# Kernel optimization log

Measured on AMD Instinct MI355X. Metric: run time of the kernel, lower is better.

## Reference

```python
import jax, jax.numpy as jnp
import numpy as np

N = 50000
E = 800000
IN, HID, OUT = 128, 128, 64


def setup_inputs() -> dict:
    key = jax.random.key(0)
    ks = jax.random.split(key, 12)
    x = jax.random.normal(ks[0], (N, IN), dtype=jnp.float32)
    src = jax.random.randint(ks[1], (E,), 0, N)
    dst = jax.random.randint(ks[2], (E,), 0, N)
    edge_index = jnp.stack([src, dst]).astype(jnp.int64)
    def lin(k, fan_in, fan_out):
        s = 1.0 / np.sqrt(fan_in)
        return jax.random.uniform(k, (fan_in, fan_out), jnp.float32, -s, s)
    return {
        "x": x,
        "edge_index": edge_index,
        "w_l0": lin(ks[3], IN, HID), "b0": jnp.zeros((HID,), jnp.float32), "w_r0": lin(ks[4], IN, HID),
        "w_l1": lin(ks[5], HID, HID), "b1": jnp.zeros((HID,), jnp.float32), "w_r1": lin(ks[6], HID, HID),
        "w_l2": lin(ks[7], HID, OUT), "b2": jnp.zeros((OUT,), jnp.float32), "w_r2": lin(ks[8], HID, OUT),
    }


def _sage_conv(x, src, dst, w_l, b, w_r, num_nodes):
    # mean aggregation of source features onto destination nodes
    msg = x[src]                                            # [E, d]
    summed = jax.ops.segment_sum(msg, dst, num_segments=num_nodes)  # [N, d]
    deg = jax.ops.segment_sum(jnp.ones((src.shape[0],), x.dtype), dst, num_segments=num_nodes)
    aggr = summed / jnp.maximum(deg, 1.0)[:, None]
    # out = lin_l(aggr) + lin_r(x_root); bias only on lin_l (PyG SAGEConv default)
    return aggr @ w_l + b + x @ w_r


def reference(x, edge_index, w_l0, b0, w_r0, w_l1, b1, w_r1, w_l2, b2, w_r2):
    src, dst = edge_index[0].astype(jnp.int32), edge_index[1].astype(jnp.int32)
    n = x.shape[0]
    h = jax.nn.relu(_sage_conv(x, src, dst, w_l0, b0, w_r0, n))  # dropout: eval mode -> identity
    h = jax.nn.relu(_sage_conv(h, src, dst, w_l1, b1, w_r1, n))
    return _sage_conv(h, src, dst, w_l2, b2, w_r2, n)
```

## Files before the change

kernel.cpp:

```cpp
#include <hip/hip_runtime.h>
#include <cstdint>
#include <cstddef>


#define HID 128
#define NSLICE 8
#define FILL_BLOCKS_PER_SLICE 256
#define FILL_BLOCKS (NSLICE * FILL_BLOCKS_PER_SLICE)
#define GEMM_BLOCKS 1024
#define CAP 64

using short8 = __attribute__((ext_vector_type(8))) short;
using f32x4  = __attribute__((ext_vector_type(4))) float;


__device__ __forceinline__ unsigned short f32_to_bf16(float f)
{
    union { float f; unsigned int i; } c; c.f = f;
    const unsigned int x = c.i;
    const unsigned int r = x + 0x7fffu + ((x >> 16) & 1u);
    return (unsigned short)(r >> 16);
}

__device__ __forceinline__ float bf16_hi_to_f32(unsigned int hi16_in_low)
{
    union { unsigned int i; float f; } c; c.i = hi16_in_low << 16;
    return c.f;
}

__device__ __forceinline__ unsigned int pack_bf16(float a, float b)
{
    return ((unsigned int)f32_to_bf16(b) << 16) | (unsigned int)f32_to_bf16(a);
}


#define PREP_THREADS (2 * 2 * HID * HID + 2 * 64 * HID)

__global__ __launch_bounds__(256) void prep_wt_zero_kernel(
    const float* __restrict__ wl0, const float* __restrict__ wr0,
    const float* __restrict__ wl1, const float* __restrict__ wr1,
    const float* __restrict__ wl2, const float* __restrict__ wr2,
    unsigned short* __restrict__ wt0, unsigned short* __restrict__ wt1,
    unsigned short* __restrict__ wt2, int* __restrict__ deg, int n)
{
    const int idx = blockIdx.x * 256 + threadIdx.x;
    const int per128 = 2 * HID * HID;
    if (idx < per128) {
        const int k = idx & (HID - 1), c = idx >> 7;
        const float v = (c < HID) ? wl0[(size_t)k * HID + c] : wr0[(size_t)k * HID + (c - HID)];
        wt0[idx] = f32_to_bf16(v);
    } else if (idx < 2 * per128) {
        const int j = idx - per128;
        const int k = j & (HID - 1), c = j >> 7;
        const float v = (c < HID) ? wl1[(size_t)k * HID + c] : wr1[(size_t)k * HID + (c - HID)];
        wt1[j] = f32_to_bf16(v);
    } else if (idx < PREP_THREADS) {
        const int j = idx - 2 * per128;
        const int k = j & (HID - 1), c = j >> 7;
        const float v = (c < 64) ? wl2[(size_t)k * 64 + c] : wr2[(size_t)k * 64 + (c - 64)];
        wt2[j] = f32_to_bf16(v);
    } else {
        const int j = idx - PREP_THREADS;
        if (j < n) deg[j] = 0;
    }
}


__global__ __launch_bounds__(256) void bucket_fill_sliced_kernel(
    const int* __restrict__ src, const int* __restrict__ dst,
    int* __restrict__ deg, unsigned short* __restrict__ esrc, int E, int n)
{
    const int slice = blockIdx.x & (NSLICE - 1);
    const int nps   = (n + NSLICE - 1) / NSLICE;
    const int lo    = slice * nps;
    const unsigned span = (unsigned)(min(lo + nps, n) - lo);
    const int stride = FILL_BLOCKS_PER_SLICE * 256;
    const int nq = E >> 2;

    for (int q = (blockIdx.x >> 3) * 256 + threadIdx.x; q < nq; q += stride) {
        const int4 d4 = ((const int4*)dst)[q];
        const bool p0 = (unsigned)(d4.x - lo) < span;
        const bool p1 = (unsigned)(d4.y - lo) < span;
        const bool p2 = (unsigned)(d4.z - lo) < span;
        const bool p3 = (unsigned)(d4.w - lo) < span;
        if (p0 | p1 | p2 | p3) {
            const int4 s4 = ((const int4*)src)[q];
            if (p0 && (unsigned)s4.x < (unsigned)n) {
                const int p = atomicAdd(&deg[d4.x], 1);
                if (p < CAP) esrc[(size_t)d4.x * CAP + p] = (unsigned short)s4.x;
            }
            if (p1 && (unsigned)s4.y < (unsigned)n) {
                const int p = atomicAdd(&deg[d4.y], 1);
                if (p < CAP) esrc[(size_t)d4.y * CAP + p] = (unsigned short)s4.y;
            }
            if (p2 && (unsigned)s4.z < (unsigned)n) {
                const int p = atomicAdd(&deg[d4.z], 1);
                if (p < CAP) esrc[(size_t)d4.z * CAP + p] = (unsigned short)s4.z;
            }
            if (p3 && (unsigned)s4.w < (unsigned)n) {
                const int p = atomicAdd(&deg[d4.w], 1);
                if (p < CAP) esrc[(size_t)d4.w * CAP + p] = (unsigned short)s4.w;
            }
        }
    }
    if ((blockIdx.x >> 3) == 0 && slice == 0) {
        for (int e = (nq << 2) + threadIdx.x; e < E; e += 256) {
            const int d = dst[e];
            const int s = src[e];
            if ((unsigned)d < (unsigned)n && (unsigned)s < (unsigned)n) {
                const int p = atomicAdd(&deg[d], 1);
                if (p < CAP) esrc[(size_t)d * CAP + p] = (unsigned short)s;
            }
        }
    }
}


template <int DOUT, bool IN_F32, bool R_BF16>
__global__ __launch_bounds__(256) void sage_mfma_gemm(
    const void* __restrict__ hin,
    const unsigned short* __restrict__ wtc,
    const float* __restrict__ bias,
    unsigned short* __restrict__ p, void* __restrict__ r, int n)
{
    constexpr int CPW = (2 * DOUT) / 64;

    const int tx   = threadIdx.x;
    const int wv   = tx >> 6;
    const int lane = tx & 63;
    const int quad = lane >> 4;
    const int l15  = lane & 15;

    short8 B[CPW][4];
#pragma unroll
    for (int t = 0; t < CPW; ++t) {
        const int c = (wv * CPW + t) * 16 + l15;
#pragma unroll
        for (int q = 0; q < 4; ++q)
            B[t][q] = *(const short8*)(wtc + (size_t)c * HID + q * 32 + quad * 8);
    }

    const int slabs = (n + 15) >> 4;
    for (int slab = blockIdx.x; slab < slabs; slab += gridDim.x) {
        const int r0 = slab * 16;
        const int rr = min(r0 + l15, n - 1);

        short8 A[4];
        if (IN_F32) {
            const float* hf = (const float*)hin;
#pragma unroll
            for (int q = 0; q < 4; ++q) {
                const float4 f0 = *(const float4*)(hf + (size_t)rr * HID + q * 32 + quad * 8);
                const float4 f1 = *(const float4*)(hf + (size_t)rr * HID + q * 32 + quad * 8 + 4);
                short8 a;
                a[0] = (short)f32_to_bf16(f0.x); a[1] = (short)f32_to_bf16(f0.y);
                a[2] = (short)f32_to_bf16(f0.z); a[3] = (short)f32_to_bf16(f0.w);
                a[4] = (short)f32_to_bf16(f1.x); a[5] = (short)f32_to_bf16(f1.y);
                a[6] = (short)f32_to_bf16(f1.z); a[7] = (short)f32_to_bf16(f1.w);
                A[q] = a;
            }
        } else {
            const unsigned short* hb = (const unsigned short*)hin;
#pragma unroll
            for (int q = 0; q < 4; ++q)
                A[q] = *(const short8*)(hb + (size_t)rr * HID + q * 32 + quad * 8);
        }

        f32x4 acc[CPW];
#pragma unroll
        for (int t = 0; t < CPW; ++t) acc[t] = (f32x4){0.f, 0.f, 0.f, 0.f};
#pragma unroll
        for (int q = 0; q < 4; ++q)
#pragma unroll
            for (int t = 0; t < CPW; ++t)
                acc[t] = __builtin_amdgcn_mfma_f32_16x16x32_bf16(A[q], B[t][q], acc[t], 0, 0, 0);

#pragma unroll
        for (int t = 0; t < CPW; ++t) {
            const int c0  = (wv * CPW + t) * 16;
            const int col = c0 + l15;
            if (c0 < DOUT) {
#pragma unroll
                for (int i = 0; i < 4; ++i) {
                    const int row = r0 + quad * 4 + i;
                    if (row < n) p[(size_t)row * DOUT + col] = f32_to_bf16(acc[t][i]);
                }
            } else {
                const float bv = bias[col - DOUT];
#pragma unroll
                for (int i = 0; i < 4; ++i) {
                    const int row = r0 + quad * 4 + i;
                    if (row < n) {
                        const float v = acc[t][i] + bv;
                        if (R_BF16)
                            ((unsigned short*)r)[(size_t)row * DOUT + (col - DOUT)] = f32_to_bf16(v);
                        else
                            ((float*)r)[(size_t)row * DOUT + (col - DOUT)] = v;
                    }
                }
            }
        }
    }
}


template <int DOUT, bool RELU, bool OUTBF16, bool R_BF16>
__global__ __launch_bounds__(256) void sage_post_aggregate(
    const unsigned short* __restrict__ p, const void* __restrict__ r,
    const int* __restrict__ deg, const unsigned short* __restrict__ esrc,
    void* __restrict__ out, int n)
{
    const int wid  = threadIdx.x >> 6;
    const int lane = threadIdx.x & 63;
    const int node = blockIdx.x * 4 + wid;
    if (node >= n) return;
    const int dg   = deg[node];
    const int degc = min(dg, CAP);
    const float inv = 1.0f / fmaxf((float)dg, 1.0f);

    const int sidx = (int)esrc[(size_t)node * CAP + lane];

    if constexpr (DOUT == 128) {
        const int g  = lane >> 4;
        const int lo = lane & 15;
        float acc[4][8];
#pragma unroll
        for (int j = 0; j < 4; ++j)
#pragma unroll
            for (int c = 0; c < 8; ++c) acc[j][c] = 0.f;

        for (int e0 = 0; e0 < degc; e0 += 16) {
#pragma unroll
            for (int j = 0; j < 4; ++j) {
                const int slot = e0 + j * 4 + g;
                const float w  = (slot < degc) ? 1.0f : 0.0f;
                const int s    = __shfl(sidx, min(slot, degc - 1), 64);
                const short8 v = *(const short8*)(p + (size_t)s * DOUT + lo * 8);
#pragma unroll
                for (int c = 0; c < 8; ++c)
                    acc[j][c] = fmaf(w, bf16_hi_to_f32((unsigned short)v[c]), acc[j][c]);
            }
        }
        float s8[8];
#pragma unroll
        for (int c = 0; c < 8; ++c) {
            float t = (acc[0][c] + acc[1][c]) + (acc[2][c] + acc[3][c]);
            t += __shfl_xor(t, 16, 64);
            t += __shfl_xor(t, 32, 64);
            s8[c] = t * inv;
        }
        if (g == 0) {
            float rc[8];
            if (R_BF16) {
                const short8 rv = *(const short8*)((const unsigned short*)r + (size_t)node * DOUT + lo * 8);
#pragma unroll
                for (int c = 0; c < 8; ++c) rc[c] = bf16_hi_to_f32((unsigned short)rv[c]);
            } else {
                const float4 q0 = *(const float4*)((const float*)r + (size_t)node * DOUT + lo * 8);
                const float4 q1 = *(const float4*)((const float*)r + (size_t)node * DOUT + lo * 8 + 4);
                rc[0] = q0.x; rc[1] = q0.y; rc[2] = q0.z; rc[3] = q0.w;
                rc[4] = q1.x; rc[5] = q1.y; rc[6] = q1.z; rc[7] = q1.w;
            }
            float o[8];
#pragma unroll
            for (int c = 0; c < 8; ++c) {
                o[c] = s8[c] + rc[c];
                if (RELU) o[c] = fmaxf(o[c], 0.f);
            }
            if (OUTBF16) {
                uint4 st;
                st.x = pack_bf16(o[0], o[1]); st.y = pack_bf16(o[2], o[3]);
                st.z = pack_bf16(o[4], o[5]); st.w = pack_bf16(o[6], o[7]);
                *(uint4*)((unsigned short*)out + (size_t)node * DOUT + lo * 8) = st;
            } else {
                float4 s0, s1;
                s0.x = o[0]; s0.y = o[1]; s0.z = o[2]; s0.w = o[3];
                s1.x = o[4]; s1.y = o[5]; s1.z = o[6]; s1.w = o[7];
                *(float4*)((float*)out + (size_t)node * DOUT + lo * 8) = s0;
                *(float4*)((float*)out + (size_t)node * DOUT + lo * 8 + 4) = s1;
            }
        }
    } else {
        const int g  = lane >> 3;
        const int lo = lane & 7;
        float acc[2][8];
#pragma unroll
        for (int j = 0; j < 2; ++j)
#pragma unroll
            for (int c = 0; c < 8; ++c) acc[j][c] = 0.f;

        for (int e0 = 0; e0 < degc; e0 += 16) {
#pragma unroll
            for (int j = 0; j < 2; ++j) {
                const int slot = e0 + j * 8 + g;
                const float w  = (slot < degc) ? 1.0f : 0.0f;
                const int s    = __shfl(sidx, min(slot, degc - 1), 64);
                const short8 v = *(const short8*)(p + (size_t)s * DOUT + lo * 8);
#pragma unroll
                for (int c = 0; c < 8; ++c)
                    acc[j][c] = fmaf(w, bf16_hi_to_f32((unsigned short)v[c]), acc[j][c]);
            }
        }
        float s8[8];
#pragma unroll
        for (int c = 0; c < 8; ++c) {
            float t = acc[0][c] + acc[1][c];
            t += __shfl_xor(t, 8, 64);
            t += __shfl_xor(t, 16, 64);
            t += __shfl_xor(t, 32, 64);
            s8[c] = t * inv;
        }
        if (g == 0) {
            float rc[8];
            if (R_BF16) {
                const short8 rv = *(const short8*)((const unsigned short*)r + (size_t)node * DOUT + lo * 8);
#pragma unroll
                for (int c = 0; c < 8; ++c) rc[c] = bf16_hi_to_f32((unsigned short)rv[c]);
            } else {
                const float4 q0 = *(const float4*)((const float*)r + (size_t)node * DOUT + lo * 8);
                const float4 q1 = *(const float4*)((const float*)r + (size_t)node * DOUT + lo * 8 + 4);
                rc[0] = q0.x; rc[1] = q0.y; rc[2] = q0.z; rc[3] = q0.w;
                rc[4] = q1.x; rc[5] = q1.y; rc[6] = q1.z; rc[7] = q1.w;
            }
            float o[8];
#pragma unroll
            for (int c = 0; c < 8; ++c) {
                o[c] = s8[c] + rc[c];
                if (RELU) o[c] = fmaxf(o[c], 0.f);
            }
            if (OUTBF16) {
                uint4 st;
                st.x = pack_bf16(o[0], o[1]); st.y = pack_bf16(o[2], o[3]);
                st.z = pack_bf16(o[4], o[5]); st.w = pack_bf16(o[6], o[7]);
                *(uint4*)((unsigned short*)out + (size_t)node * DOUT + lo * 8) = st;
            } else {
                float4 s0, s1;
                s0.x = o[0]; s0.y = o[1]; s0.z = o[2]; s0.w = o[3];
                s1.x = o[4]; s1.y = o[5]; s1.z = o[6]; s1.w = o[7];
                *(float4*)((float*)out + (size_t)node * DOUT + lo * 8) = s0;
                *(float4*)((float*)out + (size_t)node * DOUT + lo * 8 + 4) = s1;
            }
        }
    }
}


static inline size_t align_up(size_t v, size_t a) { return (v + a - 1) & ~(a - 1); }

extern "C" void kernel_launch(void* const* d_in, const int* in_sizes, int n_in,
                              void* d_out, int out_size, void* d_ws, size_t ws_size,
                              hipStream_t stream)
{
    const float* x   = (const float*)d_in[0];
    const int*   ei  = (const int*)d_in[1];
    const float* wl0 = (const float*)d_in[2];
    const float* b0  = (const float*)d_in[3];
    const float* wr0 = (const float*)d_in[4];
    const float* wl1 = (const float*)d_in[5];
    const float* b1  = (const float*)d_in[6];
    const float* wr1 = (const float*)d_in[7];
    const float* wl2 = (const float*)d_in[8];
    const float* b2  = (const float*)d_in[9];
    const float* wr2 = (const float*)d_in[10];
    float*       out = (float*)d_out;

    const int N = in_sizes[0] / HID;
    const int E = in_sizes[1] / 2;
    const int* src = ei;
    const int* dst = ei + E;

    char*  ws  = (char*)d_ws;
    size_t off = 0;
    int* deg      = (int*)(ws + off); off = align_up(off + (size_t)N * 4, 256);
    unsigned short* esrc = (unsigned short*)(ws + off); off = align_up(off + (size_t)N * CAP * 2, 256);
    unsigned short* pbuf = (unsigned short*)(ws + off); off = align_up(off + (size_t)N * HID * 2, 256);
    unsigned short* rb16 = (unsigned short*)(ws + off); off = align_up(off + (size_t)N * HID * 2, 256);
    float* rbf32  = (float*)(ws + off); off = align_up(off + (size_t)N * HID * 4, 256);
    unsigned short* hbf = (unsigned short*)(ws + off); off = align_up(off + (size_t)N * HID * 2, 256);
    unsigned short* wt0 = (unsigned short*)(ws + off); off = align_up(off + (size_t)2 * HID * HID * 2, 256);
    unsigned short* wt1 = (unsigned short*)(ws + off); off = align_up(off + (size_t)2 * HID * HID * 2, 256);
    unsigned short* wt2 = (unsigned short*)(ws + off); off = align_up(off + (size_t)HID * HID * 2, 256);
    (void)ws_size; (void)n_in; (void)out_size;

    prep_wt_zero_kernel<<<(PREP_THREADS + N + 255) / 256, 256, 0, stream>>>(
        wl0, wr0, wl1, wr1, wl2, wr2, wt0, wt1, wt2, deg, N);

    bucket_fill_sliced_kernel<<<FILL_BLOCKS, 256, 0, stream>>>(
        src, dst, deg, esrc, E, N);

    const int aggGrid = (N + 3) / 4;

    sage_mfma_gemm<128, true, true><<<GEMM_BLOCKS, 256, 0, stream>>>(x, wt0, b0, pbuf, rb16, N);
    sage_post_aggregate<128, true, true, true><<<aggGrid, 256, 0, stream>>>(pbuf, rb16, deg, esrc, hbf, N);

    sage_mfma_gemm<128, false, true><<<GEMM_BLOCKS, 256, 0, stream>>>(hbf, wt1, b1, pbuf, rb16, N);
    sage_post_aggregate<128, true, true, true><<<aggGrid, 256, 0, stream>>>(pbuf, rb16, deg, esrc, hbf, N);

    sage_mfma_gemm<64, false, false><<<GEMM_BLOCKS, 256, 0, stream>>>(hbf, wt2, b2, pbuf, rbf32, N);
    sage_post_aggregate<64, false, false, false><<<aggGrid, 256, 0, stream>>>(pbuf, rbf32, deg, esrc, out, N);
}
```

Before: 285.2 us.

## Fuse the three SAGE layers into one cooperative persistent kernel with grid syncs

Replaces the six separate GEMM and aggregation launches with a single cooperative kernel. The kernel runs the gemm and aggregate bodies as grid-stride loops and separates the stages with grid.sync(). This removes five kernel launch gaps and tail effects. In exchange, the grid is capped by occupancy (at most 2048 blocks), so the aggregation, which used 12500 blocks, loses parallelism and latency hiding, and every grid barrier adds its own cost. A fallback to the original launches is kept for when the cooperative launch fails.

After: 678.9 us. +138.0%, slower.

```diff
diff --git a/kernel.cpp b/kernel.cpp
--- a/kernel.cpp
+++ b/kernel.cpp
@@ -1,6 +1,9 @@
 #include <hip/hip_runtime.h>
+#include <hip/hip_cooperative_groups.h>
 #include <cstdint>
 #include <cstddef>
+
+namespace cg = cooperative_groups;
 
 
 #define HID 128
@@ -117,9 +120,9 @@
 
 
 template <int DOUT, bool IN_F32, bool R_BF16>
-__global__ __launch_bounds__(256) void sage_mfma_gemm(
-    const void* __restrict__ hin,
-    const unsigned short* __restrict__ wtc,
+__device__ __forceinline__ void gemm_body(
+    int bid, int nblk,
+    const void* __restrict__ hin, const unsigned short* __restrict__ wtc,
     const float* __restrict__ bias,
     unsigned short* __restrict__ p, void* __restrict__ r, int n)
 {
@@ -141,7 +144,7 @@
     }
 
     const int slabs = (n + 15) >> 4;
-    for (int slab = blockIdx.x; slab < slabs; slab += gridDim.x) {
+    for (int slab = bid; slab < slabs; slab += nblk) {
         const int r0 = slab * 16;
         const int rr = min(r0 + l15, n - 1);
 
@@ -203,6 +206,157 @@
     }
 }
 
+template <int DOUT, bool IN_F32, bool R_BF16>
+__global__ __launch_bounds__(256) void sage_mfma_gemm(
+    const void* __restrict__ hin, const unsigned short* __restrict__ wtc,
+    const float* __restrict__ bias,
+    unsigned short* __restrict__ p, void* __restrict__ r, int n)
+{
+    gemm_body<DOUT, IN_F32, R_BF16>(blockIdx.x, gridDim.x, hin, wtc, bias, p, r, n);
+}
+
+
+template <int DOUT, bool RELU, bool OUTBF16, bool R_BF16>
+__device__ __forceinline__ void agg_body(
+    int bid, int nblk,
+    const unsigned short* __restrict__ p, const void* __restrict__ r,
+    const int* __restrict__ deg, const unsigned short* __restrict__ esrc,
+    void* __restrict__ out, int n)
+{
+    const int wid  = threadIdx.x >> 6;
+    const int lane = threadIdx.x & 63;
+
+    for (int node = bid * 4 + wid; node < n; node += nblk * 4) {
+        const int dg   = deg[node];
+        const int degc = min(dg, CAP);
+        const float inv = 1.0f / fmaxf((float)dg, 1.0f);
+
+        const int sidx = (int)esrc[(size_t)node * CAP + lane];
+
+        if constexpr (DOUT == 128) {
+            const int g  = lane >> 4;
+            const int lo = lane & 15;
+            float acc[4][8];
+#pragma unroll
+            for (int j = 0; j < 4; ++j)
+#pragma unroll
+                for (int c = 0; c < 8; ++c) acc[j][c] = 0.f;
+
+            for (int e0 = 0; e0 < degc; e0 += 16) {
+#pragma unroll
+                for (int j = 0; j < 4; ++j) {
+                    const int slot = e0 + j * 4 + g;
+                    const float w  = (slot < degc) ? 1.0f : 0.0f;
+                    const int s    = __shfl(sidx, min(slot, degc - 1), 64);
+                    const short8 v = *(const short8*)(p + (size_t)s * DOUT + lo * 8);
+#pragma unroll
+                    for (int c = 0; c < 8; ++c)
+                        acc[j][c] = fmaf(w, bf16_hi_to_f32((unsigned short)v[c]), acc[j][c]);
+                }
+            }
+            float s8[8];
+#pragma unroll
+            for (int c = 0; c < 8; ++c) {
+                float t = (acc[0][c] + acc[1][c]) + (acc[2][c] + acc[3][c]);
+                t += __shfl_xor(t, 16, 64);
+                t += __shfl_xor(t, 32, 64);
+                s8[c] = t * inv;
+            }
+            if (g == 0) {
+                float rc[8];
+                if (R_BF16) {
+                    const short8 rv = *(const short8*)((const unsigned short*)r + (size_t)node * DOUT + lo * 8);
+#pragma unroll
+                    for (int c = 0; c < 8; ++c) rc[c] = bf16_hi_to_f32((unsigned short)rv[c]);
+                } else {
+                    const float4 q0 = *(const float4*)((const float*)r + (size_t)node * DOUT + lo * 8);
+                    const float4 q1 = *(const float4*)((const float*)r + (size_t)node * DOUT + lo * 8 + 4);
+                    rc[0] = q0.x; rc[1] = q0.y; rc[2] = q0.z; rc[3] = q0.w;
+                    rc[4] = q1.x; rc[5] = q1.y; rc[6] = q1.z; rc[7] = q1.w;
+                }
+                float o[8];
+#pragma unroll
+                for (int c = 0; c < 8; ++c) {
+                    o[c] = s8[c] + rc[c];
+                    if (RELU) o[c] = fmaxf(o[c], 0.f);
+                }
+                if (OUTBF16) {
+                    uint4 st;
+                    st.x = pack_bf16(o[0], o[1]); st.y = pack_bf16(o[2], o[3]);
+                    st.z = pack_bf16(o[4], o[5]); st.w = pack_bf16(o[6], o[7]);
+                    *(uint4*)((unsigned short*)out + (size_t)node * DOUT + lo * 8) = st;
+                } else {
+                    float4 s0, s1;
+                    s0.x = o[0]; s0.y = o[1]; s0.z = o[2]; s0.w = o[3];
+                    s1.x = o[4]; s1.y = o[5]; s1.z = o[6]; s1.w = o[7];
+                    *(float4*)((float*)out + (size_t)node * DOUT + lo * 8) = s0;
+                    *(float4*)((float*)out + (size_t)node * DOUT + lo * 8 + 4) = s1;
+                }
+            }
+        } else {
+            const int g  = lane >> 3;
+            const int lo = lane & 7;
+            float acc[2][8];
+#pragma unroll
+            for (int j = 0; j < 2; ++j)
+#pragma unroll
+                for (int c = 0; c < 8; ++c) acc[j][c] = 0.f;
+
+            for (int e0 = 0; e0 < degc; e0 += 16) {
+#pragma unroll
+                for (int j = 0; j < 2; ++j) {
+                    const int slot = e0 + j * 8 + g;
+                    const float w  = (slot < degc) ? 1.0f : 0.0f;
+                    const int s    = __shfl(sidx, min(slot, degc - 1), 64);
+                    const short8 v = *(const short8*)(p + (size_t)s * DOUT + lo * 8);
+#pragma unroll
+                    for (int c = 0; c < 8; ++c)
+                        acc[j][c] = fmaf(w, bf16_hi_to_f32((unsigned short)v[c]), acc[j][c]);
+                }
+            }
+            float s8[8];
+#pragma unroll
+            for (int c = 0; c < 8; ++c) {
+                float t = acc[0][c] + acc[1][c];
+                t += __shfl_xor(t, 8, 64);
+                t += __shfl_xor(t, 16, 64);
+                t += __shfl_xor(t, 32, 64);
+                s8[c] = t * inv;
+            }
+            if (g == 0) {
+                float rc[8];
+                if (R_BF16) {
+                    const short8 rv = *(const short8*)((const unsigned short*)r + (size_t)node * DOUT + lo * 8);
+#pragma unroll
+                    for (int c = 0; c < 8; ++c) rc[c] = bf16_hi_to_f32((unsigned short)rv[c]);
+                } else {
+                    const float4 q0 = *(const float4*)((const float*)r + (size_t)node * DOUT + lo * 8);
+                    const float4 q1 = *(const float4*)((const float*)r + (size_t)node * DOUT + lo * 8 + 4);
+                    rc[0] = q0.x; rc[1] = q0.y; rc[2] = q0.z; rc[3] = q0.w;
+                    rc[4] = q1.x; rc[5] = q1.y; rc[6] = q1.z; rc[7] = q1.w;
+                }
+                float o[8];
+#pragma unroll
+                for (int c = 0; c < 8; ++c) {
+                    o[c] = s8[c] + rc[c];
+                    if (RELU) o[c] = fmaxf(o[c], 0.f);
+                }
+                if (OUTBF16) {
+                    uint4 st;
+                    st.x = pack_bf16(o[0], o[1]); st.y = pack_bf16(o[2], o[3]);
+                    st.z = pack_bf16(o[4], o[5]); st.w = pack_bf16(o[6], o[7]);
+                    *(uint4*)((unsigned short*)out + (size_t)node * DOUT + lo * 8) = st;
+                } else {
+                    float4 s0, s1;
+                    s0.x = o[0]; s0.y = o[1]; s0.z = o[2]; s0.w = o[3];
+                    s1.x = o[4]; s1.y = o[5]; s1.z = o[6]; s1.w = o[7];
+                    *(float4*)((float*)out + (size_t)node * DOUT + lo * 8) = s0;
+                    *(float4*)((float*)out + (size_t)node * DOUT + lo * 8 + 4) = s1;
+                }
+            }
+        }
+    }
+}
 
 template <int DOUT, bool RELU, bool OUTBF16, bool R_BF16>
 __global__ __launch_bounds__(256) void sage_post_aggregate(
@@ -210,138 +364,35 @@
     const int* __restrict__ deg, const unsigned short* __restrict__ esrc,
     void* __restrict__ out, int n)
 {
-    const int wid  = threadIdx.x >> 6;
-    const int lane = threadIdx.x & 63;
-    const int node = blockIdx.x * 4 + wid;
-    if (node >= n) return;
-    const int dg   = deg[node];
-    const int degc = min(dg, CAP);
-    const float inv = 1.0f / fmaxf((float)dg, 1.0f);
-
-    const int sidx = (int)esrc[(size_t)node * CAP + lane];
-
-    if constexpr (DOUT == 128) {
-        const int g  = lane >> 4;
-        const int lo = lane & 15;
-        float acc[4][8];
-#pragma unroll
-        for (int j = 0; j < 4; ++j)
-#pragma unroll
-            for (int c = 0; c < 8; ++c) acc[j][c] = 0.f;
-
-        for (int e0 = 0; e0 < degc; e0 += 16) {
-#pragma unroll
-            for (int j = 0; j < 4; ++j) {
-                const int slot = e0 + j * 4 + g;
-                const float w  = (slot < degc) ? 1.0f : 0.0f;
-                const int s    = __shfl(sidx, min(slot, degc - 1), 64);
-                const short8 v = *(const short8*)(p + (size_t)s * DOUT + lo * 8);
-#pragma unroll
-                for (int c = 0; c < 8; ++c)
-                    acc[j][c] = fmaf(w, bf16_hi_to_f32((unsigned short)v[c]), acc[j][c]);
-            }
-        }
-        float s8[8];
-#pragma unroll
-        for (int c = 0; c < 8; ++c) {
-            float t = (acc[0][c] + acc[1][c]) + (acc[2][c] + acc[3][c]);
-            t += __shfl_xor(t, 16, 64);
-            t += __shfl_xor(t, 32, 64);
-            s8[c] = t * inv;
-        }
-        if (g == 0) {
-            float rc[8];
-            if (R_BF16) {
-                const short8 rv = *(const short8*)((const unsigned short*)r + (size_t)node * DOUT + lo * 8);
-#pragma unroll
-                for (int c = 0; c < 8; ++c) rc[c] = bf16_hi_to_f32((unsigned short)rv[c]);
-            } else {
-                const float4 q0 = *(const float4*)((const float*)r + (size_t)node * DOUT + lo * 8);
-                const float4 q1 = *(const float4*)((const float*)r + (size_t)node * DOUT + lo * 8 + 4);
-                rc[0] = q0.x; rc[1] = q0.y; rc[2] = q0.z; rc[3] = q0.w;
-                rc[4] = q1.x; rc[5] = q1.y; rc[6] = q1.z; rc[7] = q1.w;
-            }
-            float o[8];
-#pragma unroll
-            for (int c = 0; c < 8; ++c) {
-                o[c] = s8[c] + rc[c];
-                if (RELU) o[c] = fmaxf(o[c], 0.f);
-            }
-            if (OUTBF16) {
-                uint4 st;
-                st.x = pack_bf16(o[0], o[1]); st.y = pack_bf16(o[2], o[3]);
-                st.z = pack_bf16(o[4], o[5]); st.w = pack_bf16(o[6], o[7]);
-                *(uint4*)((unsigned short*)out + (size_t)node * DOUT + lo * 8) = st;
-            } else {
-                float4 s0, s1;
-                s0.x = o[0]; s0.y = o[1]; s0.z = o[2]; s0.w = o[3];
-                s1.x = o[4]; s1.y = o[5]; s1.z = o[6]; s1.w = o[7];
-                *(float4*)((float*)out + (size_t)node * DOUT + lo * 8) = s0;
-                *(float4*)((float*)out + (size_t)node * DOUT + lo * 8 + 4) = s1;
-            }
-        }
-    } else {
-        const int g  = lane >> 3;
-        const int lo = lane & 7;
-        float acc[2][8];
-#pragma unroll
-        for (int j = 0; j < 2; ++j)
-#pragma unroll
-            for (int c = 0; c < 8; ++c) acc[j][c] = 0.f;
-
-        for (int e0 = 0; e0 < degc; e0 += 16) {
-#pragma unroll
-            for (int j = 0; j < 2; ++j) {
-                const int slot = e0 + j * 8 + g;
-                const float w  = (slot < degc) ? 1.0f : 0.0f;
-                const int s    = __shfl(sidx, min(slot, degc - 1), 64);
-                const short8 v = *(const short8*)(p + (size_t)s * DOUT + lo * 8);
-#pragma unroll
-                for (int c = 0; c < 8; ++c)
-                    acc[j][c] = fmaf(w, bf16_hi_to_f32((unsigned short)v[c]), acc[j][c]);
-            }
-        }
-        float s8[8];
-#pragma unroll
-        for (int c = 0; c < 8; ++c) {
-            float t = acc[0][c] + acc[1][c];
-            t += __shfl_xor(t, 8, 64);
-            t += __shfl_xor(t, 16, 64);
-            t += __shfl_xor(t, 32, 64);
-            s8[c] = t * inv;
-        }
-        if (g == 0) {
-            float rc[8];
-            if (R_BF16) {
-                const short8 rv = *(const short8*)((const unsigned short*)r + (size_t)node * DOUT + lo * 8);
-#pragma unroll
-                for (int c = 0; c < 8; ++c) rc[c] = bf16_hi_to_f32((unsigned short)rv[c]);
-            } else {
-                const float4 q0 = *(const float4*)((const float*)r + (size_t)node * DOUT + lo * 8);
-                const float4 q1 = *(const float4*)((const float*)r + (size_t)node * DOUT + lo * 8 + 4);
-                rc[0] = q0.x; rc[1] = q0.y; rc[2] = q0.z; rc[3] = q0.w;
-                rc[4] = q1.x; rc[5] = q1.y; rc[6] = q1.z; rc[7] = q1.w;
-            }
-            float o[8];
-#pragma unroll
-            for (int c = 0; c < 8; ++c) {
-                o[c] = s8[c] + rc[c];
-                if (RELU) o[c] = fmaxf(o[c], 0.f);
-            }
-            if (OUTBF16) {
-                uint4 st;
-                st.x = pack_bf16(o[0], o[1]); st.y = pack_bf16(o[2], o[3]);
-                st.z = pack_bf16(o[4], o[5]); st.w = pack_bf16(o[6], o[7]);
-                *(uint4*)((unsigned short*)out + (size_t)node * DOUT + lo * 8) = st;
-            } else {
-                float4 s0, s1;
-                s0.x = o[0]; s0.y = o[1]; s0.z = o[2]; s0.w = o[3];
-                s1.x = o[4]; s1.y = o[5]; s1.z = o[6]; s1.w = o[7];
-                *(float4*)((float*)out + (size_t)node * DOUT + lo * 8) = s0;
-                *(float4*)((float*)out + (size_t)node * DOUT + lo * 8 + 4) = s1;
-            }
-        }
-    }
+    agg_body<DOUT, RELU, OUTBF16, R_BF16>(blockIdx.x, gridDim.x, p, r, deg, esrc, out, n);
+}
+
+
+__global__ __launch_bounds__(256, 4) void sage_coop_kernel(
+    const float* __restrict__ x,
+    const unsigned short* __restrict__ wt0, const unsigned short* __restrict__ wt1,
+    const unsigned short* __restrict__ wt2,
+    const float* __restrict__ b0, const float* __restrict__ b1,
+    const float* __restrict__ b2,
+    const int* __restrict__ deg, const unsigned short* __restrict__ esrc,
+    unsigned short* __restrict__ pbuf, unsigned short* __restrict__ rb16,
+    float* __restrict__ rbf32, unsigned short* __restrict__ hbf,
+    float* __restrict__ out, int n)
+{
+    cg::grid_group grid = cg::this_grid();
+    const int bid = blockIdx.x, nblk = gridDim.x;
+
+    gemm_body<128, true, true>(bid, nblk, x, wt0, b0, pbuf, rb16, n);
+    grid.sync();
+    agg_body<128, true, true, true>(bid, nblk, pbuf, rb16, deg, esrc, hbf, n);
+    grid.sync();
+    gemm_body<128, false, true>(bid, nblk, hbf, wt1, b1, pbuf, rb16, n);
+    grid.sync();
+    agg_body<128, true, true, true>(bid, nblk, pbuf, rb16, deg, esrc, hbf, n);
+    grid.sync();
+    gemm_body<64, false, false>(bid, nblk, hbf, wt2, b2, pbuf, rbf32, n);
+    grid.sync();
+    agg_body<64, false, false, false>(bid, nblk, pbuf, rbf32, deg, esrc, out, n);
 }
 
 
@@ -364,7 +415,7 @@
     const float* wr2 = (const float*)d_in[10];
     float*       out = (float*)d_out;
 
-    const int N = in_sizes[0] / HID;
+    int N = in_sizes[0] / HID;
     const int E = in_sizes[1] / 2;
     const int* src = ei;
     const int* dst = ei + E;
@@ -388,14 +439,54 @@
     bucket_fill_sliced_kernel<<<FILL_BLOCKS, 256, 0, stream>>>(
         src, dst, deg, esrc, E, N);
 
-    const int aggGrid = (N + 3) / 4;
-
-    sage_mfma_gemm<128, true, true><<<GEMM_BLOCKS, 256, 0, stream>>>(x, wt0, b0, pbuf, rb16, N);
-    sage_post_aggregate<128, true, true, true><<<aggGrid, 256, 0, stream>>>(pbuf, rb16, deg, esrc, hbf, N);
-
-    sage_mfma_gemm<128, false, true><<<GEMM_BLOCKS, 256, 0, stream>>>(hbf, wt1, b1, pbuf, rb16, N);
-    sage_post_aggregate<128, true, true, true><<<aggGrid, 256, 0, stream>>>(pbuf, rb16, deg, esrc, hbf, N);
-
-    sage_mfma_gemm<64, false, false><<<GEMM_BLOCKS, 256, 0, stream>>>(hbf, wt2, b2, pbuf, rbf32, N);
-    sage_post_aggregate<64, false, false, false><<<aggGrid, 256, 0, stream>>>(pbuf, rbf32, deg, esrc, out, N);
-}
+    static int s_coopGrid = -2;
+    if (s_coopGrid == -2) {
+        int maxB = 0;
+        hipError_t oe = hipOccupancyMaxActiveBlocksPerMultiprocessor(
+            &maxB, sage_coop_kernel, 256, 0);
+        int nCU = 256;
+        hipDeviceProp_t props;
+        int dev = 0;
+        if (hipGetDevice(&dev) == hipSuccess &&
+            hipGetDeviceProperties(&props, dev) == hipSuccess &&
+            props.multiProcessorCount > 0)
+            nCU = props.multiProcessorCount;
+        if (oe == hipSuccess && maxB > 0) {
+            long g = (long)maxB * (long)nCU;
+            s_coopGrid = (int)(g > 2048 ? 2048 : g);
+            if (s_coopGrid < 256) s_coopGrid = 0;
+        } else {
+            s_coopGrid = 0;
+            (void)hipGetLastError();
+        }
+    }
+
+    bool coop_done = false;
+    if (s_coopGrid > 0) {
+        void* args[] = {
+            (void*)&x, (void*)&wt0, (void*)&wt1, (void*)&wt2,
+            (void*)&b0, (void*)&b1, (void*)&b2,
+            (void*)&deg, (void*)&esrc,
+            (void*)&pbuf, (void*)&rb16, (void*)&rbf32, (void*)&hbf,
+            (void*)&out, (void*)&N
+        };
+        hipError_t e = hipLaunchCooperativeKernel(
+            sage_coop_kernel, dim3(s_coopGrid), dim3(256), args, 0u, stream);
+        if (e == hipSuccess) {
+            coop_done = true;
+        } else {
+            (void)hipGetLastError();
+            s_coopGrid = 0;
+        }
+    }
+
+    if (!coop_done) {
+        const int aggGrid = (N + 3) / 4;
+        sage_mfma_gemm<128, true, true><<<GEMM_BLOCKS, 256, 0, stream>>>(x, wt0, b0, pbuf, rb16, N);
+        sage_post_aggregate<128, true, true, true><<<aggGrid, 256, 0, stream>>>(pbuf, rb16, deg, esrc, hbf, N);
+        sage_mfma_gemm<128, false, true><<<GEMM_BLOCKS, 256, 0, stream>>>(hbf, wt1, b1, pbuf, rb16, N);
+        sage_post_aggregate<128, true, true, true><<<aggGrid, 256, 0, stream>>>(pbuf, rb16, deg, esrc, hbf, N);
+        sage_mfma_gemm<64, false, false><<<GEMM_BLOCKS, 256, 0, stream>>>(hbf, wt2, b2, pbuf, rbf32, N);
+        sage_post_aggregate<64, false, false, false><<<aggGrid, 256, 0, stream>>>(pbuf, rbf32, deg, esrc, out, N);
+    }
+}
```
